# Kernel tuning notes

Measured on AMD Instinct MI355X. Metric: run time of the kernel, lower is better.

The kernel has to match this reference:

```python
import jax, jax.numpy as jnp
import numpy as np

ROWS, COLS = 4, 4
B, N = 8192, 64


def setup_inputs() -> dict:
    key = jax.random.key(0)
    k1, k2 = jax.random.split(key)
    # Scale uniform entries down so colsum(x^5)^4 stays well inside fp32 range.
    x = jax.random.uniform(k1, (B, N, N), dtype=jnp.float32) * 0.2
    # kaiming_normal_ on a (rows, cols) param: std = sqrt(2 / fan_in), fan_in = cols
    coef = jax.random.normal(k2, (ROWS, COLS), dtype=jnp.float32) * np.sqrt(2.0 / COLS)
    return {"x": x, "coef": coef}


def _forward(x, coef):
    rows, cols = coef.shape
    x = x.astype(jnp.float32)
    if x.ndim == 2:
        x = x[None]
    # Incremental matrix powers: p_i = x^(i+2), i = 0..rows-1 (the only powers
    # consumed by nout; the extra power computed in nas is dead code).
    p0 = jnp.matmul(x, x)  # x^2, [B, n, n]
    def step(p, _):
        p = jnp.matmul(x, p)
        return p, p
    if rows > 1:
        _, rest = jax.lax.scan(step, p0, None, length=rows - 1)
        powers = jnp.concatenate([p0[None], rest], axis=0)  # [rows, B, n, n]
    else:
        powers = p0[None]
    # ones[n,n] @ P has every row equal to the column sums of P, so
    # trace((ones @ P) ** (j+1)) = sum_k colsum_k(P) ** (j+1).
    colsums = powers.sum(axis=-2)  # [rows, B, n]
    exps = jnp.arange(1, cols + 1, dtype=jnp.float32)  # j + 1
    traces = jnp.sum(colsums[:, None, :, :] ** exps[None, :, None, None], axis=-1)  # [rows, cols, B]
    traces = jnp.transpose(traces, (2, 0, 1))  # [B, rows, cols]
    # nnorm: numel = rows*cols (numel of a single [rows,cols] trace matrix),
    # raised to (i + j + 2)
    pow_mat = (jnp.arange(rows, dtype=jnp.float32)[:, None]
               + jnp.arange(cols, dtype=jnp.float32)[None, :] + 2.0)
    norm = jnp.asarray(rows * cols, jnp.float32) ** pow_mat  # [rows, cols]
    return (coef * traces / norm).sum(axis=(-1, -2))  # [B]


def reference(x, coef):
    return _forward(x, coef)
```

## Files before the change

### kernel.cpp

```cpp
#include <hip/hip_runtime.h>


__device__ __forceinline__ float4 xor_reduce_rg(float4 v) {
    v.x += __shfl_xor(v.x, 16, 64); v.y += __shfl_xor(v.y, 16, 64);
    v.z += __shfl_xor(v.z, 16, 64); v.w += __shfl_xor(v.w, 16, 64);
    v.x += __shfl_xor(v.x, 32, 64); v.y += __shfl_xor(v.y, 32, 64);
    v.z += __shfl_xor(v.z, 32, 64); v.w += __shfl_xor(v.w, 32, 64);
    return v;
}

__device__ __forceinline__ float compute_batch(const float4 xr[16],
                                               const float cs[4][4], int rg) {
    float4 u = xr[0];
    #pragma unroll
    for (int k = 1; k < 16; ++k) {
        u.x += xr[k].x; u.y += xr[k].y; u.z += xr[k].z; u.w += xr[k].w;
    }
    u = xor_reduce_rg(u);

    float contrib = 0.f;
    #pragma unroll
    for (int m = 0; m < 4; ++m) {
        float4 acc = {0.f, 0.f, 0.f, 0.f};
        #pragma unroll
        for (int k = 0; k < 16; ++k) {
            const int src = 4 * rg + (k >> 2);
            const float uk = ((k & 3) == 0) ? __shfl(u.x, src, 64)
                           : ((k & 3) == 1) ? __shfl(u.y, src, 64)
                           : ((k & 3) == 2) ? __shfl(u.z, src, 64)
                           :                  __shfl(u.w, src, 64);
            acc.x += uk * xr[k].x; acc.y += uk * xr[k].y;
            acc.z += uk * xr[k].z; acc.w += uk * xr[k].w;
        }
        u = xor_reduce_rg(acc);

        #pragma unroll
        for (int c = 0; c < 4; ++c) {
            const float v1 = (c == 0) ? u.x : (c == 1) ? u.y : (c == 2) ? u.z : u.w;
            const float v2 = v1 * v1;
            const float v3 = v2 * v1;
            const float v4 = v2 * v2;
            contrib += cs[m][0] * v1 + cs[m][1] * v2 + cs[m][2] * v3 + cs[m][3] * v4;
        }
    }
    return contrib;
}

__global__ __launch_bounds__(256) void nufa_kernel(
    const float* __restrict__ x, const float* __restrict__ coef,
    float* __restrict__ out, int B)
{
    const int wave = threadIdx.x >> 6;
    const int lane = threadIdx.x & 63;
    const int b0 = (blockIdx.x * 4 + wave) * 2;
    if (b0 >= B) return;

    const int rg = lane >> 4;
    const int cg = lane & 15;

    const float4* base = reinterpret_cast<const float4*>(x)
                         + (size_t)b0 * 1024 + 256 * rg + cg;
    float4 A[16], Bv[16];
    #pragma unroll
    for (int k = 0; k < 16; ++k) A[k]  = base[16 * k];
    #pragma unroll
    for (int k = 0; k < 16; ++k) Bv[k] = base[1024 + 16 * k];

    float cs[4][4];
    #pragma unroll
    for (int i = 0; i < 4; ++i)
        #pragma unroll
        for (int j = 0; j < 4; ++j)
            cs[i][j] = coef[i * 4 + j] * (1.0f / (float)(1ull << (4 * (i + j + 2))));

    float ca = compute_batch(A,  cs, rg);
    float cb = compute_batch(Bv, cs, rg);

    #pragma unroll
    for (int d = 1; d < 16; d <<= 1) {
        ca += __shfl_xor(ca, d, 64);
        cb += __shfl_xor(cb, d, 64);
    }
    if (lane == 0) { out[b0] = ca; out[b0 + 1] = cb; }
}

extern "C" void kernel_launch(void* const* d_in, const int* in_sizes, int n_in,
                              void* d_out, int out_size, void* d_ws, size_t ws_size,
                              hipStream_t stream) {
    const float* x    = (const float*)d_in[0];
    const float* coef = (const float*)d_in[1];
    float* out        = (float*)d_out;
    const int B = in_sizes[0] / 4096;
    const int wavesNeeded = (B + 1) / 2;
    const int blocks = (wavesNeeded + 3) / 4;
    nufa_kernel<<<blocks, 256, 0, stream>>>(x, coef, out, B);
}
```

Baseline: 30.48 us.

## Split each matrix across two waves with shared-memory vector exchange

Each batch matrix was handled by a single wave, two matrices per wave. Now each matrix is split across a 128-thread block of two waves, each holding 32 rows in registers. The per-step column-sum vectors are combined through double-buffered shared memory with a block barrier at every step. This cuts per-thread register use (8 float4 instead of 32), which should raise occupancy and memory-level parallelism for this bandwidth-bound read, at the cost of five barriers per matrix and four times as many blocks.

```diff
diff --git a/kernel.cpp b/kernel.cpp
--- a/kernel.cpp
+++ b/kernel.cpp
@@ -9,22 +9,55 @@
     return v;
 }
 
-__device__ __forceinline__ float compute_batch(const float4 xr[16],
-                                               const float cs[4][4], int rg) {
-    float4 u = xr[0];
+__global__ __launch_bounds__(128, 8) void nufa_kernel(
+    const float* __restrict__ x, const float* __restrict__ coef,
+    float* __restrict__ out)
+{
+    const int w    = threadIdx.x >> 6;
+    const int lane = threadIdx.x & 63;
+    const int b    = blockIdx.x;
+    const int rg   = lane >> 4;
+    const int cg   = lane & 15;
+
+    __shared__ float4 part[2][2][16];
+
+    const float4* base = reinterpret_cast<const float4*>(x)
+                         + (size_t)b * 1024 + 512 * w + 128 * rg + cg;
+    float4 xr[8];
     #pragma unroll
-    for (int k = 1; k < 16; ++k) {
-        u.x += xr[k].x; u.y += xr[k].y; u.z += xr[k].z; u.w += xr[k].w;
+    for (int k = 0; k < 8; ++k) xr[k] = base[16 * k];
+
+    float cs[4][4];
+    #pragma unroll
+    for (int i = 0; i < 4; ++i)
+        #pragma unroll
+        for (int j = 0; j < 4; ++j)
+            cs[i][j] = coef[i * 4 + j] * (1.0f / (float)(1ull << (4 * (i + j + 2))));
+
+    float4 s = xr[0];
+    #pragma unroll
+    for (int k = 1; k < 8; ++k) {
+        s.x += xr[k].x; s.y += xr[k].y; s.z += xr[k].z; s.w += xr[k].w;
     }
-    u = xor_reduce_rg(u);
+    s = xor_reduce_rg(s);
+
+    int buf = 0;
+    if (rg == 0) part[buf][w][cg] = s;
+    __syncthreads();
+    float4 u;
+    {
+        const float4 a0 = part[buf][0][cg], a1 = part[buf][1][cg];
+        u.x = a0.x + a1.x; u.y = a0.y + a1.y; u.z = a0.z + a1.z; u.w = a0.w + a1.w;
+    }
+    buf ^= 1;
 
     float contrib = 0.f;
     #pragma unroll
     for (int m = 0; m < 4; ++m) {
         float4 acc = {0.f, 0.f, 0.f, 0.f};
         #pragma unroll
-        for (int k = 0; k < 16; ++k) {
-            const int src = 4 * rg + (k >> 2);
+        for (int k = 0; k < 8; ++k) {
+            const int src = 8 * w + 2 * rg + (k >> 2);
             const float uk = ((k & 3) == 0) ? __shfl(u.x, src, 64)
                            : ((k & 3) == 1) ? __shfl(u.y, src, 64)
                            : ((k & 3) == 2) ? __shfl(u.z, src, 64)
@@ -32,7 +65,12 @@
             acc.x += uk * xr[k].x; acc.y += uk * xr[k].y;
             acc.z += uk * xr[k].z; acc.w += uk * xr[k].w;
         }
-        u = xor_reduce_rg(acc);
+        acc = xor_reduce_rg(acc);
+        if (rg == 0) part[buf][w][cg] = acc;
+        __syncthreads();
+        const float4 a0 = part[buf][0][cg], a1 = part[buf][1][cg];
+        u.x = a0.x + a1.x; u.y = a0.y + a1.y; u.z = a0.z + a1.z; u.w = a0.w + a1.w;
+        buf ^= 1;
 
         #pragma unroll
         for (int c = 0; c < 4; ++c) {
@@ -43,45 +81,10 @@
             contrib += cs[m][0] * v1 + cs[m][1] * v2 + cs[m][2] * v3 + cs[m][3] * v4;
         }
     }
-    return contrib;
-}
-
-__global__ __launch_bounds__(256) void nufa_kernel(
-    const float* __restrict__ x, const float* __restrict__ coef,
-    float* __restrict__ out, int B)
-{
-    const int wave = threadIdx.x >> 6;
-    const int lane = threadIdx.x & 63;
-    const int b0 = (blockIdx.x * 4 + wave) * 2;
-    if (b0 >= B) return;
-
-    const int rg = lane >> 4;
-    const int cg = lane & 15;
-
-    const float4* base = reinterpret_cast<const float4*>(x)
-                         + (size_t)b0 * 1024 + 256 * rg + cg;
-    float4 A[16], Bv[16];
-    #pragma unroll
-    for (int k = 0; k < 16; ++k) A[k]  = base[16 * k];
-    #pragma unroll
-    for (int k = 0; k < 16; ++k) Bv[k] = base[1024 + 16 * k];
-
-    float cs[4][4];
-    #pragma unroll
-    for (int i = 0; i < 4; ++i)
-        #pragma unroll
-        for (int j = 0; j < 4; ++j)
-            cs[i][j] = coef[i * 4 + j] * (1.0f / (float)(1ull << (4 * (i + j + 2))));
-
-    float ca = compute_batch(A,  cs, rg);
-    float cb = compute_batch(Bv, cs, rg);
 
     #pragma unroll
-    for (int d = 1; d < 16; d <<= 1) {
-        ca += __shfl_xor(ca, d, 64);
-        cb += __shfl_xor(cb, d, 64);
-    }
-    if (lane == 0) { out[b0] = ca; out[b0 + 1] = cb; }
+    for (int d = 1; d < 16; d <<= 1) contrib += __shfl_xor(contrib, d, 64);
+    if (threadIdx.x == 0) out[b] = contrib;
 }
 
 extern "C" void kernel_launch(void* const* d_in, const int* in_sizes, int n_in,
@@ -91,7 +94,5 @@
     const float* coef = (const float*)d_in[1];
     float* out        = (float*)d_out;
     const int B = in_sizes[0] / 4096;
-    const int wavesNeeded = (B + 1) / 2;
-    const int blocks = (wavesNeeded + 3) / 4;
-    nufa_kernel<<<blocks, 256, 0, stream>>>(x, coef, out, B);
+    nufa_kernel<<<B, 128, 0, stream>>>(x, coef, out);
 }
```

New measurement: 29.98 us. Within noise of the previous version (-1.6%).

## Double-buffer batch loads across four batches per wave

Applied to the files above, without the earlier changes.

Each wave now processes four matrices instead of two and uses two register buffers, issuing the load of the next matrix before computing on the current one. The aim is to hide global memory latency behind the per-batch reduction math inside a single wave. In exchange the grid has half as many waves, which lowers the wave count available to hide latency. The conditional buffer selection may also push the compiler toward indexed register arrays or spills.

```diff
diff --git a/kernel.cpp b/kernel.cpp
--- a/kernel.cpp
+++ b/kernel.cpp
@@ -1,5 +1,7 @@
 #include <hip/hip_runtime.h>
 
+
+#define NB 4
 
 __device__ __forceinline__ float4 xor_reduce_rg(float4 v) {
     v.x += __shfl_xor(v.x, 16, 64); v.y += __shfl_xor(v.y, 16, 64);
@@ -7,6 +9,11 @@
     v.x += __shfl_xor(v.x, 32, 64); v.y += __shfl_xor(v.y, 32, 64);
     v.z += __shfl_xor(v.z, 32, 64); v.w += __shfl_xor(v.w, 32, 64);
     return v;
+}
+
+__device__ __forceinline__ void load_batch(float4 dst[16], const float4* base) {
+    #pragma unroll
+    for (int k = 0; k < 16; ++k) dst[k] = base[16 * k];
 }
 
 __device__ __forceinline__ float compute_batch(const float4 xr[16],
@@ -52,7 +59,8 @@
 {
     const int wave = threadIdx.x >> 6;
     const int lane = threadIdx.x & 63;
-    const int b0 = (blockIdx.x * 4 + wave) * 2;
+    const int w    = blockIdx.x * 4 + wave;
+    const int b0   = w * NB;
     if (b0 >= B) return;
 
     const int rg = lane >> 4;
@@ -60,11 +68,6 @@
 
     const float4* base = reinterpret_cast<const float4*>(x)
                          + (size_t)b0 * 1024 + 256 * rg + cg;
-    float4 A[16], Bv[16];
-    #pragma unroll
-    for (int k = 0; k < 16; ++k) A[k]  = base[16 * k];
-    #pragma unroll
-    for (int k = 0; k < 16; ++k) Bv[k] = base[1024 + 16 * k];
 
     float cs[4][4];
     #pragma unroll
@@ -73,15 +76,21 @@
         for (int j = 0; j < 4; ++j)
             cs[i][j] = coef[i * 4 + j] * (1.0f / (float)(1ull << (4 * (i + j + 2))));
 
-    float ca = compute_batch(A,  cs, rg);
-    float cb = compute_batch(Bv, cs, rg);
+    float4 bufA[16], bufB[16];
+    load_batch(bufA, base);
 
     #pragma unroll
-    for (int d = 1; d < 16; d <<= 1) {
-        ca += __shfl_xor(ca, d, 64);
-        cb += __shfl_xor(cb, d, 64);
+    for (int i = 0; i < NB; ++i) {
+        if (i + 1 < NB && b0 + i + 1 < B) {
+            if (i & 1) load_batch(bufA, base + (size_t)(i + 1) * 1024);
+            else       load_batch(bufB, base + (size_t)(i + 1) * 1024);
+        }
+        float c = (i & 1) ? compute_batch(bufB, cs, rg)
+                          : compute_batch(bufA, cs, rg);
+        #pragma unroll
+        for (int d = 1; d < 16; d <<= 1) c += __shfl_xor(c, d, 64);
+        if (lane == 0 && b0 + i < B) out[b0 + i] = c;
     }
-    if (lane == 0) { out[b0] = ca; out[b0 + 1] = cb; }
 }
 
 extern "C" void kernel_launch(void* const* d_in, const int* in_sizes, int n_in,
@@ -91,7 +100,7 @@
     const float* coef = (const float*)d_in[1];
     float* out        = (float*)d_out;
     const int B = in_sizes[0] / 4096;
-    const int wavesNeeded = (B + 1) / 2;
-    const int blocks = (wavesNeeded + 3) / 4;
+    const int waves  = (B + NB - 1) / NB;
+    const int blocks = (waves + 3) / 4;
     nufa_kernel<<<blocks, 256, 0, stream>>>(x, coef, out, B);
 }
```

After: 30.89 us. No clear change (+1.3%).
